# Optimization experiments

Measured on AMD Instinct MI355X. Metric: run time of the kernel, lower is better.

The kernel has to match this reference:

```python
import jax, jax.numpy as jnp
import numpy as np

B, N, C, C_OUT, E = 8, 1024, 256, 256, 16384


def setup_inputs() -> dict:
    key = jax.random.key(0)
    k1, k2, k3 = jax.random.split(key, 3)
    x = jax.random.normal(k1, (B, N, C), dtype=jnp.float32)
    edge_index = jax.random.randint(k2, (2, E, B), 0, N)  # [2, E, B], values in [0, N)
    W = jax.random.normal(k3, (C_OUT, C), dtype=jnp.float32) * 0.02  # torch Linear weight [out, in]
    b = jnp.zeros((C_OUT,), dtype=jnp.float32)
    return {"x": x, "edge_index": edge_index, "W": W, "b": b}


def reference(x, edge_index, W, b):
    Bs, Nn, Cc = x.shape
    BN = Bs * Nn
    # Vectorized version of the per-batch python loop: offset each graph's
    # node indices into the big block-diagonal adjacency.
    offs = jnp.arange(Bs, dtype=edge_index.dtype) * Nn          # [B]
    src = (edge_index[0] + offs[None, :]).reshape(-1)           # [E*B]
    dst = (edge_index[1] + offs[None, :]).reshape(-1)           # [E*B]
    adj = jnp.zeros((BN, BN), dtype=x.dtype).at[src, dst].set(1.0)
    adj = adj + jnp.eye(BN, dtype=x.dtype)                      # self loops (adds on top, as in torch code)
    D = adj.sum(axis=1)                                         # [BN]
    d_inv_sqrt = jnp.where(D > 0, jax.lax.rsqrt(D), 0.0)        # pow(-0.5) with inf -> 0
    adj_n = d_inv_sqrt[:, None] * adj * d_inv_sqrt[None, :]     # D^-1/2 A D^-1/2
    h = adj_n @ x.reshape(BN, Cc)                               # [BN, C]
    out = h @ W.T + b                                           # Linear
    return out.reshape(Bs, Nn, -1)
```

## Files before the change

kernel.cpp:

```cpp
#include <hip/hip_runtime.h>
#include <stdint.h>

#define B_   8
#define N_   1024
#define C_   256
#define E_   16384
#define BN_  (B_ * N_)
#define NW_  (N_ / 32)
#define LIST_CAP 96

typedef __attribute__((ext_vector_type(8))) short bf16x8;
typedef __attribute__((ext_vector_type(4))) float f32x4;

static __device__ __forceinline__ short f32_to_bf16(float f) {
  uint32_t u = __float_as_uint(f);
  uint32_t r = (u + 0x7fffu + ((u >> 16) & 1u)) >> 16;
  return (short)r;
}
static __device__ __forceinline__ float bf16_to_f32(short s) {
  return __uint_as_float(((uint32_t)(uint16_t)s) << 16);
}

__global__ __launch_bounds__(256) void scatter_edges(
    const int* __restrict__ ei, uint32_t* __restrict__ mask) {
  int t = blockIdx.x * 256 + threadIdx.x;
  if (t >= E_ * B_) return;
  int b   = t & (B_ - 1);
  int src = ei[t];
  int dst = ei[E_ * B_ + t];
  int row = b * N_ + src;
  atomicOr(&mask[row * NW_ + (dst >> 5)], 1u << (dst & 31));
}

__global__ __launch_bounds__(256) void gemm_bf16x3(
    const float* __restrict__ X, const float* __restrict__ W,
    const uint32_t* __restrict__ mask, float* __restrict__ Z) {
  __shared__ __attribute__((aligned(16))) short Ah[64][40];
  __shared__ __attribute__((aligned(16))) short Al[64][40];
  __shared__ __attribute__((aligned(16))) short Bh[64][40];
  __shared__ __attribute__((aligned(16))) short Bl[64][40];
  __shared__ int   dpart[4][64];
  __shared__ float dinv_s[64];

  int t  = threadIdx.x;
  int m0 = blockIdx.x * 64;
  int n0 = blockIdx.y * 64;

  {
    int row = t & 63, part = t >> 6;
    const uint4* mp =
        (const uint4*)&mask[(size_t)(m0 + row) * NW_ + part * 8];
    uint4 a = mp[0], b = mp[1];
    dpart[part][row] = __popc(a.x) + __popc(a.y) + __popc(a.z) + __popc(a.w) +
                       __popc(b.x) + __popc(b.y) + __popc(b.z) + __popc(b.w);
  }
  __syncthreads();
  if (t < 64) {
    int d = dpart[0][t] + dpart[1][t] + dpart[2][t] + dpart[3][t] + 1;
    dinv_s[t] = rsqrtf((float)d);
  }

  int lr = t >> 2;
  int lc = (t & 3) * 8;
  int wv = t >> 6;
  int ln = t & 63;
  int lm = ln & 15;
  int qd = ln >> 4;

  f32x4 acc[4];
#pragma unroll
  for (int i = 0; i < 4; i++) acc[i] = (f32x4){0.f, 0.f, 0.f, 0.f};

  for (int k0 = 0; k0 < C_; k0 += 32) {
    const float* xr = &X[(size_t)(m0 + lr) * C_ + k0 + lc];
    const float* wr = &W[(size_t)(n0 + lr) * C_ + k0 + lc];
    float xv[8], wv8[8];
    *(float4*)&xv[0] = *(const float4*)&xr[0];
    *(float4*)&xv[4] = *(const float4*)&xr[4];
    *(float4*)&wv8[0] = *(const float4*)&wr[0];
    *(float4*)&wv8[4] = *(const float4*)&wr[4];
    bf16x8 xh, xl, wh, wl;
#pragma unroll
    for (int j = 0; j < 8; j++) {
      short h = f32_to_bf16(xv[j]);
      xh[j] = h;
      xl[j] = f32_to_bf16(xv[j] - bf16_to_f32(h));
      short g = f32_to_bf16(wv8[j]);
      wh[j] = g;
      wl[j] = f32_to_bf16(wv8[j] - bf16_to_f32(g));
    }
    __syncthreads();
    *(bf16x8*)&Ah[lr][lc] = xh;
    *(bf16x8*)&Al[lr][lc] = xl;
    *(bf16x8*)&Bh[lr][lc] = wh;
    *(bf16x8*)&Bl[lr][lc] = wl;
    __syncthreads();

    bf16x8 ah = *(const bf16x8*)&Ah[16 * wv + lm][qd * 8];
    bf16x8 al = *(const bf16x8*)&Al[16 * wv + lm][qd * 8];
#pragma unroll
    for (int nt = 0; nt < 4; nt++) {
      bf16x8 bh = *(const bf16x8*)&Bh[nt * 16 + lm][qd * 8];
      bf16x8 bl = *(const bf16x8*)&Bl[nt * 16 + lm][qd * 8];
      acc[nt] = __builtin_amdgcn_mfma_f32_16x16x32_bf16(ah, bh, acc[nt], 0, 0, 0);
      acc[nt] = __builtin_amdgcn_mfma_f32_16x16x32_bf16(ah, bl, acc[nt], 0, 0, 0);
      acc[nt] = __builtin_amdgcn_mfma_f32_16x16x32_bf16(al, bh, acc[nt], 0, 0, 0);
    }
  }
  __syncthreads();

  float di[4];
#pragma unroll
  for (int r = 0; r < 4; r++) di[r] = dinv_s[16 * wv + qd * 4 + r];
#pragma unroll
  for (int nt = 0; nt < 4; nt++) {
#pragma unroll
    for (int r = 0; r < 4; r++) {
      int m = m0 + 16 * wv + qd * 4 + r;
      int n = n0 + nt * 16 + lm;
      Z[(size_t)m * C_ + n] = di[r] * acc[nt][r];
    }
  }
}

__global__ __launch_bounds__(256) void aggregate(
    const uint32_t* __restrict__ mask, const float* __restrict__ Z,
    const float* __restrict__ bias, float* __restrict__ out) {
  __shared__ uint16_t lists[4][LIST_CAP];

  int blk   = blockIdx.x;
  int batch = blk & 7;
  int group = blk >> 3;
  int wv    = threadIdx.x >> 6;
  int ln    = threadIdx.x & 63;
  int loc   = group * 4 + wv;
  int node  = batch * N_ + loc;
  int c4    = ln * 4;

  uint32_t bits = (ln < NW_) ? mask[(size_t)node * NW_ + ln] : 0u;
  int cnt = __popc(bits);
  int pfx = cnt;
#pragma unroll
  for (int off = 1; off < 64; off <<= 1) {
    int v = __shfl_up(pfx, off);
    if (ln >= off) pfx += v;
  }
  int total = __shfl(pfx, 63);
  pfx -= cnt;
  uint16_t* lst = lists[wv];
  int o = pfx, jb = ln * 32;
  while (bits) {
    int j = __ffs(bits) - 1;
    bits &= bits - 1;
    lst[o++] = (uint16_t)(jb + j);
  }
  if (ln == 0) {
    int dd = total;
    while (dd & 3) lst[dd++] = 0;
  }

  const float* zb = Z + (size_t)batch * N_ * C_;
  float4 acc = *(const float4*)&zb[(size_t)loc * C_ + c4];

  for (int k = 0; k < total; k += 4) {
    ushort4 n4 = *(const ushort4*)&lst[k];
    float4 z0 = *(const float4*)&zb[(size_t)n4.x * C_ + c4];
    float4 z1 = *(const float4*)&zb[(size_t)n4.y * C_ + c4];
    float4 z2 = *(const float4*)&zb[(size_t)n4.z * C_ + c4];
    float4 z3 = *(const float4*)&zb[(size_t)n4.w * C_ + c4];
    float w1 = (k + 1 < total) ? 1.f : 0.f;
    float w2 = (k + 2 < total) ? 1.f : 0.f;
    float w3 = (k + 3 < total) ? 1.f : 0.f;
    acc.x += z0.x; acc.y += z0.y; acc.z += z0.z; acc.w += z0.w;
    acc.x += w1 * z1.x; acc.y += w1 * z1.y; acc.z += w1 * z1.z; acc.w += w1 * z1.w;
    acc.x += w2 * z2.x; acc.y += w2 * z2.y; acc.z += w2 * z2.z; acc.w += w2 * z2.w;
    acc.x += w3 * z3.x; acc.y += w3 * z3.y; acc.z += w3 * z3.z; acc.w += w3 * z3.w;
  }

  float di = rsqrtf((float)(total + 1));
  float4 bb = *(const float4*)&bias[c4];
  float4 o4;
  o4.x = di * acc.x + bb.x;
  o4.y = di * acc.y + bb.y;
  o4.z = di * acc.z + bb.z;
  o4.w = di * acc.w + bb.w;
  *(float4*)&out[(size_t)node * C_ + c4] = o4;
}

extern "C" void kernel_launch(void* const* d_in, const int* in_sizes, int n_in,
                              void* d_out, int out_size, void* d_ws,
                              size_t ws_size, hipStream_t stream) {
  const float* x    = (const float*)d_in[0];
  const int*   ei   = (const int*)d_in[1];
  const float* W    = (const float*)d_in[2];
  const float* bias = (const float*)d_in[3];
  float*       out  = (float*)d_out;

  char* ws = (char*)d_ws;
  uint32_t* mask = (uint32_t*)(ws + 0x000000);
  float*    Z    = (float*)   (ws + 0x100000);

  hipMemsetAsync(mask, 0, (size_t)BN_ * NW_ * 4, stream);

  scatter_edges<<<(E_ * B_) / 256, 256, 0, stream>>>(ei, mask);
  gemm_bf16x3<<<dim3(BN_ / 64, C_ / 64), 256, 0, stream>>>(x, W, mask, Z);
  aggregate<<<BN_ / 4, 256, 0, stream>>>(mask, Z, bias, out);
}
```

Measured before the change: 96.32 us.

## Fuse edge scatter into GEMM and compute neighbor degree weights in aggregate

Moves the edge-to-bitmask scatter into the GEMM kernel, one edge per thread, which removes a separate launch. The GEMM no longer reads the mask to scale rows by the inverse square root of the degree. Instead, the aggregate kernel computes each neighbor's normalization weight from that neighbor's mask row popcount and applies it while summing. This removes a kernel and a dependency, at the cost of extra mask reads and shuffle reductions per neighbor in the aggregate.

```diff
diff --git a/kernel.cpp b/kernel.cpp
--- a/kernel.cpp
+++ b/kernel.cpp
@@ -21,43 +21,26 @@
   return __uint_as_float(((uint32_t)(uint16_t)s) << 16);
 }
 
-__global__ __launch_bounds__(256) void scatter_edges(
-    const int* __restrict__ ei, uint32_t* __restrict__ mask) {
-  int t = blockIdx.x * 256 + threadIdx.x;
-  if (t >= E_ * B_) return;
-  int b   = t & (B_ - 1);
-  int src = ei[t];
-  int dst = ei[E_ * B_ + t];
-  int row = b * N_ + src;
-  atomicOr(&mask[row * NW_ + (dst >> 5)], 1u << (dst & 31));
-}
-
-__global__ __launch_bounds__(256) void gemm_bf16x3(
+__global__ __launch_bounds__(256) void gemm_scatter(
     const float* __restrict__ X, const float* __restrict__ W,
-    const uint32_t* __restrict__ mask, float* __restrict__ Z) {
+    const int* __restrict__ ei, uint32_t* __restrict__ mask,
+    float* __restrict__ Y) {
   __shared__ __attribute__((aligned(16))) short Ah[64][40];
   __shared__ __attribute__((aligned(16))) short Al[64][40];
   __shared__ __attribute__((aligned(16))) short Bh[64][40];
   __shared__ __attribute__((aligned(16))) short Bl[64][40];
-  __shared__ int   dpart[4][64];
-  __shared__ float dinv_s[64];
 
   int t  = threadIdx.x;
   int m0 = blockIdx.x * 64;
   int n0 = blockIdx.y * 64;
 
   {
-    int row = t & 63, part = t >> 6;
-    const uint4* mp =
-        (const uint4*)&mask[(size_t)(m0 + row) * NW_ + part * 8];
-    uint4 a = mp[0], b = mp[1];
-    dpart[part][row] = __popc(a.x) + __popc(a.y) + __popc(a.z) + __popc(a.w) +
-                       __popc(b.x) + __popc(b.y) + __popc(b.z) + __popc(b.w);
-  }
-  __syncthreads();
-  if (t < 64) {
-    int d = dpart[0][t] + dpart[1][t] + dpart[2][t] + dpart[3][t] + 1;
-    dinv_s[t] = rsqrtf((float)d);
+    int e   = (blockIdx.y * gridDim.x + blockIdx.x) * 256 + t;
+    int b   = e & (B_ - 1);
+    int src = ei[e];
+    int dst = ei[E_ * B_ + e];
+    atomicOr(&mask[(size_t)(b * N_ + src) * NW_ + (dst >> 5)],
+             1u << (dst & 31));
   }
 
   int lr = t >> 2;
@@ -107,26 +90,23 @@
       acc[nt] = __builtin_amdgcn_mfma_f32_16x16x32_bf16(al, bh, acc[nt], 0, 0, 0);
     }
   }
-  __syncthreads();
-
-  float di[4];
-#pragma unroll
-  for (int r = 0; r < 4; r++) di[r] = dinv_s[16 * wv + qd * 4 + r];
+
 #pragma unroll
   for (int nt = 0; nt < 4; nt++) {
 #pragma unroll
     for (int r = 0; r < 4; r++) {
       int m = m0 + 16 * wv + qd * 4 + r;
       int n = n0 + nt * 16 + lm;
-      Z[(size_t)m * C_ + n] = di[r] * acc[nt][r];
+      Y[(size_t)m * C_ + n] = acc[nt][r];
     }
   }
 }
 
 __global__ __launch_bounds__(256) void aggregate(
-    const uint32_t* __restrict__ mask, const float* __restrict__ Z,
+    const uint32_t* __restrict__ mask, const float* __restrict__ Y,
     const float* __restrict__ bias, float* __restrict__ out) {
   __shared__ uint16_t lists[4][LIST_CAP];
+  __shared__ float    wgts[4][LIST_CAP];
 
   int blk   = blockIdx.x;
   int batch = blk & 7;
@@ -137,7 +117,9 @@
   int node  = batch * N_ + loc;
   int c4    = ln * 4;
 
-  uint32_t bits = (ln < NW_) ? mask[(size_t)node * NW_ + ln] : 0u;
+  const uint32_t* mb = mask + (size_t)batch * N_ * NW_;
+
+  uint32_t bits = (ln < NW_) ? mb[(size_t)loc * NW_ + ln] : 0u;
   int cnt = __popc(bits);
   int pfx = cnt;
 #pragma unroll
@@ -148,6 +130,7 @@
   int total = __shfl(pfx, 63);
   pfx -= cnt;
   uint16_t* lst = lists[wv];
+  float*    wgt = wgts[wv];
   int o = pfx, jb = ln * 32;
   while (bits) {
     int j = __ffs(bits) - 1;
@@ -156,28 +139,39 @@
   }
   if (ln == 0) {
     int dd = total;
-    while (dd & 3) lst[dd++] = 0;
-  }
-
-  const float* zb = Z + (size_t)batch * N_ * C_;
-  float4 acc = *(const float4*)&zb[(size_t)loc * C_ + c4];
+    while (dd & 3) { lst[dd] = 0; wgt[dd] = 0.f; dd++; }
+  }
+
+  int half = ln >> 5;
+  int wl   = ln & 31;
+  for (int k = 0; k < total; k += 2) {
+    int kk = k + half;
+    int nj = (kk < total) ? lst[kk] : 0;
+    int p  = __popc(mb[(size_t)nj * NW_ + wl]);
+    p += __shfl_xor(p, 1);  p += __shfl_xor(p, 2);  p += __shfl_xor(p, 4);
+    p += __shfl_xor(p, 8);  p += __shfl_xor(p, 16);
+    if (wl == 0 && kk < total) wgt[kk] = rsqrtf((float)(p + 1));
+  }
+
+  const float* yb = Y + (size_t)batch * N_ * C_;
+  float di = rsqrtf((float)(total + 1));
+  float4 s = *(const float4*)&yb[(size_t)loc * C_ + c4];
+  float4 acc;
+  acc.x = di * s.x; acc.y = di * s.y; acc.z = di * s.z; acc.w = di * s.w;
 
   for (int k = 0; k < total; k += 4) {
     ushort4 n4 = *(const ushort4*)&lst[k];
-    float4 z0 = *(const float4*)&zb[(size_t)n4.x * C_ + c4];
-    float4 z1 = *(const float4*)&zb[(size_t)n4.y * C_ + c4];
-    float4 z2 = *(const float4*)&zb[(size_t)n4.z * C_ + c4];
-    float4 z3 = *(const float4*)&zb[(size_t)n4.w * C_ + c4];
-    float w1 = (k + 1 < total) ? 1.f : 0.f;
-    float w2 = (k + 2 < total) ? 1.f : 0.f;
-    float w3 = (k + 3 < total) ? 1.f : 0.f;
-    acc.x += z0.x; acc.y += z0.y; acc.z += z0.z; acc.w += z0.w;
-    acc.x += w1 * z1.x; acc.y += w1 * z1.y; acc.z += w1 * z1.z; acc.w += w1 * z1.w;
-    acc.x += w2 * z2.x; acc.y += w2 * z2.y; acc.z += w2 * z2.z; acc.w += w2 * z2.w;
-    acc.x += w3 * z3.x; acc.y += w3 * z3.y; acc.z += w3 * z3.z; acc.w += w3 * z3.w;
-  }
-
-  float di = rsqrtf((float)(total + 1));
+    float4  w4 = *(const float4*)&wgt[k];
+    float4 z0 = *(const float4*)&yb[(size_t)n4.x * C_ + c4];
+    float4 z1 = *(const float4*)&yb[(size_t)n4.y * C_ + c4];
+    float4 z2 = *(const float4*)&yb[(size_t)n4.z * C_ + c4];
+    float4 z3 = *(const float4*)&yb[(size_t)n4.w * C_ + c4];
+    acc.x += w4.x * z0.x; acc.y += w4.x * z0.y; acc.z += w4.x * z0.z; acc.w += w4.x * z0.w;
+    acc.x += w4.y * z1.x; acc.y += w4.y * z1.y; acc.z += w4.y * z1.z; acc.w += w4.y * z1.w;
+    acc.x += w4.z * z2.x; acc.y += w4.z * z2.y; acc.z += w4.z * z2.z; acc.w += w4.z * z2.w;
+    acc.x += w4.w * z3.x; acc.y += w4.w * z3.y; acc.z += w4.w * z3.z; acc.w += w4.w * z3.w;
+  }
+
   float4 bb = *(const float4*)&bias[c4];
   float4 o4;
   o4.x = di * acc.x + bb.x;
@@ -198,11 +192,10 @@
 
   char* ws = (char*)d_ws;
   uint32_t* mask = (uint32_t*)(ws + 0x000000);
-  float*    Z    = (float*)   (ws + 0x100000);
+  float*    Y    = (float*)   (ws + 0x100000);
 
   hipMemsetAsync(mask, 0, (size_t)BN_ * NW_ * 4, stream);
 
-  scatter_edges<<<(E_ * B_) / 256, 256, 0, stream>>>(ei, mask);
-  gemm_bf16x3<<<dim3(BN_ / 64, C_ / 64), 256, 0, stream>>>(x, W, mask, Z);
-  aggregate<<<BN_ / 4, 256, 0, stream>>>(mask, Z, bias, out);
-}
+  gemm_scatter<<<dim3(BN_ / 64, C_ / 64), 256, 0, stream>>>(x, W, ei, mask, Y);
+  aggregate<<<BN_ / 4, 256, 0, stream>>>(mask, Y, bias, out);
+}
```

Result: no change. 97.29 us (+1.0%).
